# Performance work log

Measured on AMD Instinct MI355X. Metric: run time of the kernel, lower is better.

## Reference

```python
import jax, jax.numpy as jnp
import numpy as np

B, S, D = 4, 2048, 1024  # batch, seq_len, input_dimension
KD, VD = 1024, 1024      # key_dim, value_dim


def setup_inputs() -> dict:
    key = jax.random.key(0)
    ks = jax.random.split(key, 9)
    sc_in = 1.0 / np.sqrt(D)
    sc_v = 1.0 / np.sqrt(VD)
    return {
        "x":  jax.random.normal(ks[0], (B, S, D), dtype=jnp.float32),
        "Wq": jax.random.normal(ks[1], (KD, D), dtype=jnp.float32) * sc_in,
        "bq": jax.random.normal(ks[2], (KD,), dtype=jnp.float32) * 0.01,
        "Wk": jax.random.normal(ks[3], (KD, D), dtype=jnp.float32) * sc_in,
        "bk": jax.random.normal(ks[4], (KD,), dtype=jnp.float32) * 0.01,
        "Wv": jax.random.normal(ks[5], (VD, D), dtype=jnp.float32) * sc_in,
        "bv": jax.random.normal(ks[6], (VD,), dtype=jnp.float32) * 0.01,
        "Wo": jax.random.normal(ks[7], (D, VD), dtype=jnp.float32) * sc_v,
        "bo": jax.random.normal(ks[8], (D,), dtype=jnp.float32) * 0.01,
    }


def reference(x, Wq, bq, Wk, bk, Wv, bv, Wo, bo):
    # projections (torch Linear: x @ W.T + b)
    q = jnp.einsum('bsd,kd->bsk', x, Wq) + bq   # (B,S,KD)
    k = jnp.einsum('bsd,kd->bsk', x, Wk) + bk   # (B,S,KD)
    v = jnp.einsum('bsd,vd->bsv', x, Wv) + bv   # (B,S,VD)

    scores = jnp.einsum('bqk,bsk->bqs', q, k) / jnp.sqrt(jnp.float32(KD))  # (B,S,S)

    # sign rescale: scores * sign(scores) (sign(0) mapped to 1) == |scores| with zeros kept
    sign_mask = jnp.sign(scores)
    sign_mask = sign_mask + (sign_mask == 0).astype(jnp.float32)

    # causal mask: lower-triangular (incl diag) multiplied by 1, strict upper -> -inf
    seq = scores.shape[-1]
    causal = jnp.tril(jnp.ones((seq, seq), dtype=bool))
    masked = jnp.where(causal, scores * sign_mask, -jnp.inf)

    weights = jax.nn.softmax(masked, axis=2)            # (B,S,S)
    out = jnp.einsum('bqs,bsv->bqv', weights, v)        # (B,S,VD)
    return jnp.einsum('bqv,dv->bqd', out, Wo) + bo      # (B,S,D)
```

## Files before the change

### kernel.cpp

```cpp
#include <hip/hip_runtime.h>
#include <hip/hip_bf16.h>
#include <cstdint>


#define BM 128
#define BN 128

typedef __attribute__((ext_vector_type(8))) __bf16 bf16x8;
typedef __attribute__((ext_vector_type(4))) __bf16 bf16x4;
typedef __attribute__((ext_vector_type(4))) float floatx4;

struct Bias3 { const float* b[3]; };
struct Ptr4 { const float* p[4]; };

__device__ __forceinline__ void async_copy16(const __bf16* g, const __bf16* l) {
  __builtin_amdgcn_global_load_lds(
      (const __attribute__((address_space(1))) unsigned int*)(const void*)g,
      (__attribute__((address_space(3))) unsigned int*)(unsigned)(uintptr_t)(const void*)l,
      16, 0, 0);
}

__device__ __forceinline__ void gemm_core(const __bf16* __restrict__ pA,
                                          const __bf16* __restrict__ pB,
                                          int K, int kSteps64, int mb, int nb,
                                          floatx4 (&acc)[4][4]) {
  __shared__ __align__(16) __bf16 As0[BM * 32];
  __shared__ __align__(16) __bf16 As1[BM * 32];
  __shared__ __align__(16) __bf16 Bs0[BN * 32];
  __shared__ __align__(16) __bf16 Bs1[BN * 32];

  const int t = threadIdx.x;
  const int lane = t & 63;
  const int wave = t >> 6;
  const int quad = lane >> 4;
  const int l16 = lane & 15;
  const int wm = wave >> 1;
  const int wn = wave & 1;

  const __bf16* gA = pA + (long)(mb * BM + (t >> 2)) * K + ((t & 3) * 8);
  const __bf16* gB = pB + (long)(nb * BN + (t >> 2)) * K + ((t & 3) * 8);
  const long rowHalf = (long)64 * K;
  __bf16* lA0 = &As0[t * 8];
  __bf16* lA1 = &As1[t * 8];
  __bf16* lB0 = &Bs0[t * 8];
  __bf16* lB1 = &Bs1[t * 8];

  for (int kk = 0; kk < kSteps64; ++kk) {
    const long ko = (long)kk * 64;
    async_copy16(gA + ko, lA0);
    async_copy16(gA + ko + rowHalf, lA0 + 2048);
    async_copy16(gA + ko + 32, lA1);
    async_copy16(gA + ko + 32 + rowHalf, lA1 + 2048);
    async_copy16(gB + ko, lB0);
    async_copy16(gB + ko + rowHalf, lB0 + 2048);
    async_copy16(gB + ko + 32, lB1);
    async_copy16(gB + ko + 32 + rowHalf, lB1 + 2048);
    __syncthreads();

#pragma unroll
    for (int p = 0; p < 2; ++p) {
      const __bf16* As = p ? As1 : As0;
      const __bf16* Bs = p ? Bs1 : Bs0;
      bf16x8 af[4], bfr[4];
#pragma unroll
      for (int i = 0; i < 4; ++i) {
        af[i] = *(const bf16x8*)&As[(wm * 64 + i * 16 + l16) * 32 + quad * 8];
        bfr[i] = *(const bf16x8*)&Bs[(wn * 64 + i * 16 + l16) * 32 + quad * 8];
      }
#pragma unroll
      for (int i = 0; i < 4; ++i)
#pragma unroll
        for (int j = 0; j < 4; ++j)
          acc[i][j] = __builtin_amdgcn_mfma_f32_16x16x32_bf16(af[i], bfr[j],
                                                              acc[i][j], 0, 0, 0);
    }
    __syncthreads();
  }
}

__global__ void __launch_bounds__(256, 2)
gemm_qkv(const __bf16* __restrict__ xb, const __bf16* __restrict__ Wqkv,
         Bias3 bias, __bf16* __restrict__ qk, __bf16* __restrict__ Vt,
         int S, int D, int KD, int B) {
  const int id = blockIdx.x;
  const int xcd = id & 7;
  const int j = id >> 3;
  const int mb = xcd * 8 + (j & 7);
  const int rest = j >> 3;
  const int nb = rest & 7;
  const int z = rest >> 3;

  floatx4 acc[4][4] = {};
  gemm_core(xb, Wqkv + (long)z * KD * D, D, D / 64, mb, nb, acc);

  const int t = threadIdx.x;
  const int lane = t & 63, wave = t >> 6;
  const int rb = (wave >> 1) * 64 + (lane >> 4) * 4;
  const int cb = (wave & 1) * 64 + (lane & 15);
  const float* bz = bias.b[z];

  if (z < 2) {
    __bf16* C = qk + (long)z * B * S * KD;
#pragma unroll
    for (int j4 = 0; j4 < 4; ++j4) {
      const int gc = nb * BN + cb + j4 * 16;
      const float bv = bz[gc];
#pragma unroll
      for (int i = 0; i < 4; ++i) {
        const int gr = mb * BM + rb + i * 16;
#pragma unroll
        for (int r = 0; r < 4; ++r)
          C[(long)(gr + r) * KD + gc] = (__bf16)(acc[i][j4][r] + bv);
      }
    }
  } else {
    const int bb = (mb * BM) / S;
    const int s0 = mb * BM - bb * S;
#pragma unroll
    for (int j4 = 0; j4 < 4; ++j4) {
      const int gc = nb * BN + cb + j4 * 16;
      const float bv = bz[gc];
#pragma unroll
      for (int i = 0; i < 4; ++i) {
        const int sr = s0 + rb + i * 16;
        bf16x4 o;
#pragma unroll
        for (int r = 0; r < 4; ++r) o[r] = (__bf16)(acc[i][j4][r] + bv);
        *(bf16x4*)&Vt[((long)bb * KD + gc) * S + sr] = o;
      }
    }
  }
}

__global__ void __launch_bounds__(256, 2)
gemm_scores(const __bf16* __restrict__ q, const __bf16* __restrict__ k,
            __bf16* __restrict__ P, float* __restrict__ lsum, int S, int KD) {
  const int id = blockIdx.x;
  const int xcd = id & 7;
  const int j = id >> 3;
  const int nb = j & 15;
  const int comb = j >> 4;
  const int b = comb >> 1;
  const int mb = (comb & 1) ? (15 - xcd) : xcd;
  if (nb > mb) return;

  floatx4 acc[4][4] = {};
  gemm_core(q + (long)b * S * KD, k + (long)b * S * KD, KD, KD / 64, mb, nb, acc);

  const int t = threadIdx.x;
  const int lane = t & 63, wave = t >> 6;
  const int l16 = lane & 15;
  const int rb = (wave >> 1) * 64 + (lane >> 4) * 4;
  const int cb = (wave & 1) * 64 + l16;
  __bf16* C = P + (long)b * S * S;
  float* lrow = lsum + (long)b * S;
  const float sc = 0.03125f;

#pragma unroll
  for (int i = 0; i < 4; ++i) {
#pragma unroll
    for (int r = 0; r < 4; ++r) {
      const int row = mb * BM + rb + i * 16 + r;
      float psum = 0.f;
#pragma unroll
      for (int j4 = 0; j4 < 4; ++j4) {
        const int col = nb * BN + cb + j4 * 16;
        const float p = (col <= row) ? __expf(fabsf(acc[i][j4][r] * sc)) : 0.f;
        psum += p;
        C[(long)row * S + col] = (__bf16)p;
      }
      psum += __shfl_xor(psum, 1, 64);
      psum += __shfl_xor(psum, 2, 64);
      psum += __shfl_xor(psum, 4, 64);
      psum += __shfl_xor(psum, 8, 64);
      if (l16 == 0) atomicAdd(&lrow[row], psum);
    }
  }
}

__global__ void __launch_bounds__(256, 2)
gemm_pv(const __bf16* __restrict__ P, const __bf16* __restrict__ Vt,
        const float* __restrict__ lsum, __bf16* __restrict__ O, int S, int VD) {
  const int id = blockIdx.x;
  const int xcd = id & 7;
  const int j = id >> 3;
  const int nb = j & 7;
  const int comb = j >> 3;
  const int b = comb >> 1;
  const int mb = (comb & 1) ? (15 - xcd) : xcd;

  floatx4 acc[4][4] = {};
  gemm_core(P + (long)b * S * S, Vt + (long)b * VD * S, S, (mb + 1) * 2, mb, nb,
            acc);

  const int t = threadIdx.x;
  const int lane = t & 63, wave = t >> 6;
  const int rb = (wave >> 1) * 64 + (lane >> 4) * 4;
  const int cb = (wave & 1) * 64 + (lane & 15);
  const float* lrow = lsum + (long)b * S;

#pragma unroll
  for (int i = 0; i < 4; ++i) {
#pragma unroll
    for (int r = 0; r < 4; ++r) {
      const int row = mb * BM + rb + i * 16 + r;
      const float inv = 1.f / lrow[row];
#pragma unroll
      for (int j4 = 0; j4 < 4; ++j4) {
        const int col = nb * BN + cb + j4 * 16;
        O[((long)b * S + row) * VD + col] = (__bf16)(acc[i][j4][r] * inv);
      }
    }
  }
}

__global__ void __launch_bounds__(256, 2)
gemm_out(const __bf16* __restrict__ O, const __bf16* __restrict__ Wob,
         const float* __restrict__ bo, float* __restrict__ out, int M, int N,
         int K) {
  const int id = blockIdx.x;
  const int xcd = id & 7;
  const int j = id >> 3;
  const int mb = xcd * 8 + (j & 7);
  const int nb = j >> 3;

  floatx4 acc[4][4] = {};
  gemm_core(O, Wob, K, K / 64, mb, nb, acc);

  const int t = threadIdx.x;
  const int lane = t & 63, wave = t >> 6;
  const int rb = (wave >> 1) * 64 + (lane >> 4) * 4;
  const int cb = (wave & 1) * 64 + (lane & 15);

#pragma unroll
  for (int j4 = 0; j4 < 4; ++j4) {
    const int gc = nb * BN + cb + j4 * 16;
    const float bv = bo[gc];
#pragma unroll
    for (int i = 0; i < 4; ++i) {
      const int gr = mb * BM + rb + i * 16;
#pragma unroll
      for (int r = 0; r < 4; ++r) out[(long)(gr + r) * N + gc] = acc[i][j4][r] + bv;
    }
  }
}

__global__ void prep(const float* __restrict__ x, Ptr4 wp,
                     __bf16* __restrict__ xb, __bf16* __restrict__ Wb,
                     float* __restrict__ lsum) {
  const int bid = blockIdx.x;
  const int t = threadIdx.x;
  if (bid < 8192) {
    const long i = ((long)bid * 256 + t) * 4;
    const float4 f = *(const float4*)(x + i);
    bf16x4 o;
    o[0] = (__bf16)f.x; o[1] = (__bf16)f.y; o[2] = (__bf16)f.z; o[3] = (__bf16)f.w;
    *(bf16x4*)(xb + i) = o;
  } else if (bid < 12288) {
    const int slot = (bid - 8192) * 256 + t;
    const int which = slot >> 18;
    const long e = (long)(slot & 0x3ffff) * 4;
    const float4 f = *(const float4*)(wp.p[which] + e);
    bf16x4 o;
    o[0] = (__bf16)f.x; o[1] = (__bf16)f.y; o[2] = (__bf16)f.z; o[3] = (__bf16)f.w;
    *(bf16x4*)(Wb + ((long)which << 20) + e) = o;
  } else {
#pragma unroll
    for (int e = 0; e < 8; ++e)
      *(float4*)(lsum + (e * 256 + t) * 4) = float4{0.f, 0.f, 0.f, 0.f};
  }
}

extern "C" void kernel_launch(void* const* d_in, const int* in_sizes, int n_in,
                              void* d_out, int out_size, void* d_ws, size_t ws_size,
                              hipStream_t stream) {
  const float* x = (const float*)d_in[0];
  const float* Wq = (const float*)d_in[1];
  const float* bq = (const float*)d_in[2];
  const float* Wk = (const float*)d_in[3];
  const float* bk = (const float*)d_in[4];
  const float* Wv = (const float*)d_in[5];
  const float* bv = (const float*)d_in[6];
  const float* Wo = (const float*)d_in[7];
  const float* bo = (const float*)d_in[8];
  float* out = (float*)d_out;

  constexpr int B = 4, S = 2048, D = 1024, KD = 1024, VD = 1024;
  constexpr long MB_ = 1024 * 1024;

  char* w = (char*)d_ws;
  __bf16* xb = (__bf16*)(w);
  __bf16* qk = (__bf16*)(w + 16 * MB_);
  __bf16* Vt = (__bf16*)(w + 48 * MB_);
  __bf16* P  = (__bf16*)(w + 64 * MB_);
  __bf16* Wb = (__bf16*)(w + 96 * MB_);
  float* lsum = (float*)(w + 104 * MB_);
  __bf16* O = xb;

  Ptr4 wp{{Wq, Wk, Wv, Wo}};
  prep<<<12289, 256, 0, stream>>>(x, wp, xb, Wb, lsum);

  Bias3 b3{{bq, bk, bv}};
  gemm_qkv<<<1536, 256, 0, stream>>>(xb, Wb, b3, qk, Vt, S, D, KD, B);

  gemm_scores<<<1024, 256, 0, stream>>>(qk, qk + (long)B * S * KD, P, lsum, S, KD);

  gemm_pv<<<512, 256, 0, stream>>>(P, Vt, lsum, O, S, VD);

  gemm_out<<<512, 256, 0, stream>>>(O, Wb + 3l * D * VD, bo, out, B * S, D, VD);
}
```

Measured before the change: 264.4 us.

## Fold output projection into value weights to drop the final GEMM

```diff
diff --git a/kernel.cpp b/kernel.cpp
--- a/kernel.cpp
+++ b/kernel.cpp
@@ -10,8 +10,9 @@
 typedef __attribute__((ext_vector_type(4))) __bf16 bf16x4;
 typedef __attribute__((ext_vector_type(4))) float floatx4;
 
-struct Bias3 { const float* b[3]; };
-struct Ptr4 { const float* p[4]; };
+struct WPtr3 { const __bf16* w[3]; };
+struct BPtr3 { const float* b[3]; };
+struct Ptr3 { const float* p[3]; };
 
 __device__ __forceinline__ void async_copy16(const __bf16* g, const __bf16* l) {
   __builtin_amdgcn_global_load_lds(
@@ -79,8 +80,33 @@
 }
 
 __global__ void __launch_bounds__(256, 2)
-gemm_qkv(const __bf16* __restrict__ xb, const __bf16* __restrict__ Wqkv,
-         Bias3 bias, __bf16* __restrict__ qk, __bf16* __restrict__ Vt,
+gemm_wvo(const __bf16* __restrict__ Wob, const __bf16* __restrict__ Wvt,
+         __bf16* __restrict__ Wvo) {
+  const int id = blockIdx.x;
+  const int mb = id >> 3, nb = id & 7;
+  floatx4 acc[4][4] = {};
+  gemm_core(Wob, Wvt, 1024, 16, mb, nb, acc);
+
+  const int t = threadIdx.x;
+  const int lane = t & 63, wave = t >> 6;
+  const int rb = (wave >> 1) * 64 + (lane >> 4) * 4;
+  const int cb = (wave & 1) * 64 + (lane & 15);
+#pragma unroll
+  for (int j4 = 0; j4 < 4; ++j4) {
+    const int gc = nb * BN + cb + j4 * 16;
+#pragma unroll
+    for (int i = 0; i < 4; ++i) {
+      const int gr = mb * BM + rb + i * 16;
+#pragma unroll
+      for (int r = 0; r < 4; ++r)
+        Wvo[(long)(gr + r) * 1024 + gc] = (__bf16)acc[i][j4][r];
+    }
+  }
+}
+
+__global__ void __launch_bounds__(256, 2)
+gemm_qku(const __bf16* __restrict__ xb, WPtr3 wgt, BPtr3 bias,
+         __bf16* __restrict__ qk, __bf16* __restrict__ Ut,
          int S, int D, int KD, int B) {
   const int id = blockIdx.x;
   const int xcd = id & 7;
@@ -91,7 +117,7 @@
   const int z = rest >> 3;
 
   floatx4 acc[4][4] = {};
-  gemm_core(xb, Wqkv + (long)z * KD * D, D, D / 64, mb, nb, acc);
+  gemm_core(xb, wgt.w[z], D, D / 64, mb, nb, acc);
 
   const int t = threadIdx.x;
   const int lane = t & 63, wave = t >> 6;
@@ -126,7 +152,7 @@
         bf16x4 o;
 #pragma unroll
         for (int r = 0; r < 4; ++r) o[r] = (__bf16)(acc[i][j4][r] + bv);
-        *(bf16x4*)&Vt[((long)bb * KD + gc) * S + sr] = o;
+        *(bf16x4*)&Ut[((long)bb * D + gc) * S + sr] = o;
       }
     }
   }
@@ -179,8 +205,9 @@
 }
 
 __global__ void __launch_bounds__(256, 2)
-gemm_pv(const __bf16* __restrict__ P, const __bf16* __restrict__ Vt,
-        const float* __restrict__ lsum, __bf16* __restrict__ O, int S, int VD) {
+gemm_pvo(const __bf16* __restrict__ P, const __bf16* __restrict__ Ut,
+         const float* __restrict__ lsum, const float* __restrict__ bo,
+         float* __restrict__ out, int S, int D) {
   const int id = blockIdx.x;
   const int xcd = id & 7;
   const int j = id >> 3;
@@ -190,7 +217,7 @@
   const int mb = (comb & 1) ? (15 - xcd) : xcd;
 
   floatx4 acc[4][4] = {};
-  gemm_core(P + (long)b * S * S, Vt + (long)b * VD * S, S, (mb + 1) * 2, mb, nb,
+  gemm_core(P + (long)b * S * S, Ut + (long)b * D * S, S, (mb + 1) * 2, mb, nb,
             acc);
 
   const int t = threadIdx.x;
@@ -208,46 +235,19 @@
 #pragma unroll
       for (int j4 = 0; j4 < 4; ++j4) {
         const int col = nb * BN + cb + j4 * 16;
-        O[((long)b * S + row) * VD + col] = (__bf16)(acc[i][j4][r] * inv);
-      }
-    }
-  }
-}
-
-__global__ void __launch_bounds__(256, 2)
-gemm_out(const __bf16* __restrict__ O, const __bf16* __restrict__ Wob,
-         const float* __restrict__ bo, float* __restrict__ out, int M, int N,
-         int K) {
-  const int id = blockIdx.x;
-  const int xcd = id & 7;
-  const int j = id >> 3;
-  const int mb = xcd * 8 + (j & 7);
-  const int nb = j >> 3;
-
-  floatx4 acc[4][4] = {};
-  gemm_core(O, Wob, K, K / 64, mb, nb, acc);
-
-  const int t = threadIdx.x;
-  const int lane = t & 63, wave = t >> 6;
-  const int rb = (wave >> 1) * 64 + (lane >> 4) * 4;
-  const int cb = (wave & 1) * 64 + (lane & 15);
-
-#pragma unroll
-  for (int j4 = 0; j4 < 4; ++j4) {
-    const int gc = nb * BN + cb + j4 * 16;
-    const float bv = bo[gc];
-#pragma unroll
-    for (int i = 0; i < 4; ++i) {
-      const int gr = mb * BM + rb + i * 16;
-#pragma unroll
-      for (int r = 0; r < 4; ++r) out[(long)(gr + r) * N + gc] = acc[i][j4][r] + bv;
-    }
-  }
-}
-
-__global__ void prep(const float* __restrict__ x, Ptr4 wp,
+        out[((long)b * S + row) * D + col] = acc[i][j4][r] * inv + bo[col];
+      }
+    }
+  }
+}
+
+__global__ void prep(const float* __restrict__ x, Ptr3 wp,
+                     const float* __restrict__ Wv, const float* __restrict__ bv,
                      __bf16* __restrict__ xb, __bf16* __restrict__ Wb,
+                     __bf16* __restrict__ Wvt, float* __restrict__ bvo,
                      float* __restrict__ lsum) {
+  __shared__ __bf16 tile[64][66];
+  __shared__ float wsum[4];
   const int bid = blockIdx.x;
   const int t = threadIdx.x;
   if (bid < 8192) {
@@ -256,7 +256,7 @@
     bf16x4 o;
     o[0] = (__bf16)f.x; o[1] = (__bf16)f.y; o[2] = (__bf16)f.z; o[3] = (__bf16)f.w;
     *(bf16x4*)(xb + i) = o;
-  } else if (bid < 12288) {
+  } else if (bid < 11264) {
     const int slot = (bid - 8192) * 256 + t;
     const int which = slot >> 18;
     const long e = (long)(slot & 0x3ffff) * 4;
@@ -264,6 +264,32 @@
     bf16x4 o;
     o[0] = (__bf16)f.x; o[1] = (__bf16)f.y; o[2] = (__bf16)f.z; o[3] = (__bf16)f.w;
     *(bf16x4*)(Wb + ((long)which << 20) + e) = o;
+  } else if (bid < 11520) {
+    const int idx = bid - 11264;
+    const int r0 = (idx >> 4) * 64, c0 = (idx & 15) * 64;
+#pragma unroll
+    for (int e = 0; e < 16; ++e) {
+      const int i = e * 256 + t;
+      const int r = i >> 6, c = i & 63;
+      tile[r][c] = (__bf16)Wv[(long)(r0 + r) * 1024 + (c0 + c)];
+    }
+    __syncthreads();
+#pragma unroll
+    for (int e = 0; e < 16; ++e) {
+      const int i = e * 256 + t;
+      const int r = i >> 6, c = i & 63;
+      Wvt[(long)(c0 + r) * 1024 + (r0 + c)] = tile[c][r];
+    }
+  } else if (bid < 12544) {
+    const int d = bid - 11520;
+    const float* row = wp.p[2] + (long)d * 1024;
+    float s = 0.f;
+    for (int v = t; v < 1024; v += 256) s += bv[v] * row[v];
+#pragma unroll
+    for (int off = 32; off > 0; off >>= 1) s += __shfl_down(s, off, 64);
+    if ((t & 63) == 0) wsum[t >> 6] = s;
+    __syncthreads();
+    if (t == 0) bvo[d] = wsum[0] + wsum[1] + wsum[2] + wsum[3];
   } else {
 #pragma unroll
     for (int e = 0; e < 8; ++e)
@@ -285,27 +311,34 @@
   const float* bo = (const float*)d_in[8];
   float* out = (float*)d_out;
 
-  constexpr int B = 4, S = 2048, D = 1024, KD = 1024, VD = 1024;
+  constexpr int B = 4, S = 2048, D = 1024, KD = 1024;
   constexpr long MB_ = 1024 * 1024;
 
   char* w = (char*)d_ws;
   __bf16* xb = (__bf16*)(w);
   __bf16* qk = (__bf16*)(w + 16 * MB_);
-  __bf16* Vt = (__bf16*)(w + 48 * MB_);
+  __bf16* Ut = (__bf16*)(w + 48 * MB_);
   __bf16* P  = (__bf16*)(w + 64 * MB_);
   __bf16* Wb = (__bf16*)(w + 96 * MB_);
-  float* lsum = (float*)(w + 104 * MB_);
-  __bf16* O = xb;
-
-  Ptr4 wp{{Wq, Wk, Wv, Wo}};
-  prep<<<12289, 256, 0, stream>>>(x, wp, xb, Wb, lsum);
-
-  Bias3 b3{{bq, bk, bv}};
-  gemm_qkv<<<1536, 256, 0, stream>>>(xb, Wb, b3, qk, Vt, S, D, KD, B);
+  __bf16* Wvt = (__bf16*)(w + 102 * MB_);
+  __bf16* Wvo = (__bf16*)(w + 104 * MB_);
+  float* lsum = (float*)(w + 106 * MB_);
+  float* bvo = (float*)(w + 106 * MB_ + 65536);
+
+  __bf16* Wqb = Wb;
+  __bf16* Wkb = Wb + (1l << 20);
+  __bf16* Wob = Wb + (2l << 20);
+
+  Ptr3 wp{{Wq, Wk, Wo}};
+  prep<<<12545, 256, 0, stream>>>(x, wp, Wv, bv, xb, Wb, Wvt, bvo, lsum);
+
+  gemm_wvo<<<64, 256, 0, stream>>>(Wob, Wvt, Wvo);
+
+  WPtr3 w3{{Wqb, Wkb, Wvo}};
+  BPtr3 b3{{bq, bk, bvo}};
+  gemm_qku<<<1536, 256, 0, stream>>>(xb, w3, b3, qk, Ut, S, D, KD, B);
 
   gemm_scores<<<1024, 256, 0, stream>>>(qk, qk + (long)B * S * KD, P, lsum, S, KD);
 
-  gemm_pv<<<512, 256, 0, stream>>>(P, Vt, lsum, O, S, VD);
-
-  gemm_out<<<512, 256, 0, stream>>>(O, Wb + 3l * D * VD, bo, out, B * S, D, VD);
-}
+  gemm_pvo<<<512, 256, 0, stream>>>(P, Ut, lsum, bo, out, S, D);
+}
```

Result: no change. 261.0 us (-1.3%).
